# Kernel optimization log

Measured on AMD Instinct MI355X. Metric: run time of the kernel, lower is better.

## Reference

```python
import jax, jax.numpy as jnp
import numpy as np
from jax import lax

BN_EPS = 1e-5


def _conv(x, w):
    # stride-1, VALID conv; the torch 'locally connected' layer shares weights
    # across pixels, so it is exactly a standard conv2d.
    return lax.conv_general_dilated(
        x, w, window_strides=(1, 1), padding='VALID',
        dimension_numbers=('NCHW', 'OIHW', 'NCHW'))


def _batchnorm(x, gamma, beta):
    # training-mode BatchNorm2d: batch statistics over (N, H, W)
    mean = jnp.mean(x, axis=(0, 2, 3), keepdims=True)
    var = jnp.var(x, axis=(0, 2, 3), keepdims=True)
    xhat = (x - mean) * lax.rsqrt(var + BN_EPS)
    return xhat * gamma[None, :, None, None] + beta[None, :, None, None]


def setup_inputs() -> dict:
    key = jax.random.key(0)
    ks = jax.random.split(key, 6)
    B = 16384
    x = jax.random.normal(ks[0], (B, 256), dtype=jnp.float32)
    w1 = jax.random.normal(ks[1], (16, 1, 3, 3), dtype=jnp.float32)
    w2 = jax.random.normal(ks[2], (32, 16, 2, 2), dtype=jnp.float32)
    w3 = jax.random.normal(ks[3], (64, 32, 1, 1), dtype=jnp.float32)
    fan_in = 64 * 13 * 13
    bound = 1.0 / np.sqrt(fan_in)
    fc_w = jax.random.uniform(ks[4], (10, fan_in), minval=-bound, maxval=bound, dtype=jnp.float32)
    fc_b = jax.random.uniform(ks[5], (10,), minval=-bound, maxval=bound, dtype=jnp.float32)
    return {
        'x': x, 'w1': w1, 'w2': w2, 'w3': w3,
        'g1': jnp.ones((16,), jnp.float32), 'b1': jnp.zeros((16,), jnp.float32),
        'g2': jnp.ones((32,), jnp.float32), 'b2': jnp.zeros((32,), jnp.float32),
        'g3': jnp.ones((64,), jnp.float32), 'b3': jnp.zeros((64,), jnp.float32),
        'fc_w': fc_w, 'fc_b': fc_b,
    }


def reference(x, w1, w2, w3, g1, b1, g2, b2, g3, b3, fc_w, fc_b):
    h = x.reshape(-1, 1, 16, 16)                     # [B,1,16,16]
    h = jax.nn.relu(_batchnorm(_conv(h, w1), g1, b1))  # [B,16,14,14]
    h = jax.nn.relu(_batchnorm(_conv(h, w2), g2, b2))  # [B,32,13,13]
    h = jax.nn.relu(_batchnorm(_conv(h, w3), g3, b3))  # [B,64,13,13]
    h = h.reshape(h.shape[0], -1)                    # [B, 64*13*13]
    # dropout is identity in eval/deterministic mode
    return h @ fc_w.T + fc_b                         # [B,10]
```

## Files before the change

kernel.cpp:

```cpp
#include <hip/hip_runtime.h>


#define NPART 1024
#define P1_OFF 0
#define P2_OFF 32768
#define ST_OFF 229376
#define ST1 ST_OFF
#define ST2 (ST_OFF + 32)
#define ST3 (ST_OFF + 96)
#define C2R_OFF 230400
#define C2P_OFF 262144
#define A2G_BYTE 5242880ull
#define FCB_N (13 * 8192)
#define A1S 24
#define A1B 384
#define A3P 1048

typedef __attribute__((ext_vector_type(8))) short bf16x8;
typedef __attribute__((ext_vector_type(4))) float f32x4;

__device__ __forceinline__ unsigned int f2bf(float f) {
  unsigned int u = __float_as_uint(f);
  return (u + 0x7fffu + ((u >> 16) & 1u)) >> 16;
}
__device__ __forceinline__ unsigned int pkbf(float a, float b) {
  unsigned ua = __float_as_uint(a) + 0x8000u;
  unsigned ub = __float_as_uint(b) + 0x8000u;
  return __builtin_amdgcn_perm(ub, ua, 0x07060302u);
}
__device__ __forceinline__ short cvtbf(float a) {
  return (short)((__float_as_uint(a) + 0x8000u) >> 16);
}

__device__ __forceinline__ void conv1_mfma(
    const float* __restrict__ sxi,
    short* ph_buf,
    int r, int b, int q, bf16x8 b1f, float rs1, float rt1)
{
  bf16x8 af = {0, 0, 0, 0, 0, 0, 0, 0};
  unsigned* au = (unsigned*)&af;
  if (q == 0) {
    au[0] = pkbf(sxi[r * 16 + b],        sxi[r * 16 + b + 1]);
    au[1] = pkbf(sxi[r * 16 + b + 2],    sxi[(r + 1) * 16 + b]);
    au[2] = pkbf(sxi[(r + 1) * 16 + b + 1], sxi[(r + 1) * 16 + b + 2]);
    au[3] = pkbf(sxi[(r + 2) * 16 + b],  sxi[(r + 2) * 16 + b + 1]);
  } else if (q == 1) {
    au[0] = pkbf(sxi[(r + 2) * 16 + b + 2], 0.f);
  }
  f32x4 acc = {0.f, 0.f, 0.f, 0.f};
  acc = __builtin_amdgcn_mfma_f32_16x16x32_bf16(af, b1f, acc, 0, 0, 0);
  short* ph = ph_buf + (r & 1) * A1B;
#pragma unroll
  for (int rr = 0; rr < 4; ++rr) {
    float v = rs1 * acc[rr] + rt1;
    v = v > 0.f ? v : 0.f;
    ph[(4 * q + rr) * A1S + b] = cvtbf(v);
  }
}

__device__ __forceinline__ bf16x8 conv1_bfrag(const float* w1, int b, int q) {
  bf16x8 v;
#pragma unroll
  for (int j = 0; j < 8; ++j) {
    int tap = 8 * q + j;
    v[j] = (tap < 9) ? (short)f2bf(w1[b * 9 + tap]) : (short)0;
  }
  return v;
}

__global__ __launch_bounds__(256) void k1_xstats(
    const float* __restrict__ x, float* __restrict__ ws)
{
  __shared__ float sx[32 * 256];
  __shared__ float redl[4 * 56];
  const int tid = threadIdx.x, w = tid >> 6, lane = tid & 63;
  {
    const float4* xs = (const float4*)(x + (size_t)blockIdx.x * (32 * 256));
    float4* sd = (float4*)sx;
    for (int e = tid; e < 32 * 64; e += 256) sd[e] = xs[e];
  }
  __syncthreads();
  float S[9], C[45];
#pragma unroll
  for (int a = 0; a < 9; ++a) S[a] = 0.f;
#pragma unroll
  for (int a = 0; a < 45; ++a) C[a] = 0.f;
  for (int p = tid; p < 32 * 196; p += 256) {
    int img = p / 196, rem = p - img * 196;
    int i = rem / 14, j = rem - i * 14;
    const float* px = sx + img * 256 + i * 16 + j;
    float v[9];
    v[0] = px[0];  v[1] = px[1];  v[2] = px[2];
    v[3] = px[16]; v[4] = px[17]; v[5] = px[18];
    v[6] = px[32]; v[7] = px[33]; v[8] = px[34];
    int idx = 0;
#pragma unroll
    for (int a = 0; a < 9; ++a) {
      S[a] += v[a];
#pragma unroll
      for (int c = a; c < 9; ++c) { C[idx] += v[a] * v[c]; ++idx; }
    }
  }
#pragma unroll
  for (int a = 0; a < 9; ++a) {
    float v = S[a];
#pragma unroll
    for (int d = 1; d < 64; d <<= 1) v += __shfl_xor(v, d);
    if (lane == 0) redl[w * 56 + a] = v;
  }
#pragma unroll
  for (int a = 0; a < 45; ++a) {
    float v = C[a];
#pragma unroll
    for (int d = 1; d < 64; d <<= 1) v += __shfl_xor(v, d);
    if (lane == 0) redl[w * 56 + 9 + a] = v;
  }
  __syncthreads();
  if (tid < 54)
    ws[P1_OFF + blockIdx.x * 54 + tid] =
        redl[tid] + redl[56 + tid] + redl[112 + tid] + redl[168 + tid];
}

__global__ __launch_bounds__(256) void k_stats1(
    const float* __restrict__ w1, const float* __restrict__ gamma,
    const float* __restrict__ beta, float* __restrict__ ws)
{
  __shared__ float part[216];
  __shared__ float acc[54];
  const int tid = threadIdx.x;
  if (tid < 216) {
    int a = tid >> 2, seg = tid & 3;
    float s = 0.f;
    for (int i = seg * 128; i < seg * 128 + 128; ++i)
      s += ws[P1_OFF + i * 54 + a];
    part[tid] = s;
  }
  __syncthreads();
  if (tid < 54)
    acc[tid] = part[tid * 4] + part[tid * 4 + 1] +
               part[tid * 4 + 2] + part[tid * 4 + 3];
  __syncthreads();
  if (tid < 16) {
    float wr[9];
#pragma unroll
    for (int p = 0; p < 9; ++p) wr[p] = w1[tid * 9 + p];
    float msum = 0.f;
#pragma unroll
    for (int p = 0; p < 9; ++p) msum += wr[p] * acc[p];
    float e2 = 0.f;
    int idx = 9;
#pragma unroll
    for (int a = 0; a < 9; ++a)
#pragma unroll
      for (int c = a; c < 9; ++c) {
        float t = wr[a] * wr[c] * acc[idx];
        e2 += (c == a) ? t : 2.f * t;
        ++idx;
      }
    const float inv_n = 1.0f / (16384.0f * 196.0f);
    float mean = msum * inv_n;
    float var  = e2 * inv_n - mean * mean;
    float sv   = gamma[tid] * rsqrtf(var + 1e-5f);
    ws[ST1 + tid]      = sv;
    ws[ST1 + 16 + tid] = beta[tid] - mean * sv;
  }
}

__global__ __launch_bounds__(256) void k_stats2(
    const float* __restrict__ gamma, const float* __restrict__ beta,
    float* __restrict__ ws, int nch, int part_off, int st_off, float inv_n)
{
  const int c = blockIdx.x, tid = threadIdx.x;
  const int w = tid >> 6, lane = tid & 63;
  __shared__ float rs[4], rq[4];
  float s = 0.f, q = 0.f;
#pragma unroll 4
  for (int i = tid; i < NPART; i += 256) {
    s += ws[part_off + i * 2 * nch + c];
    q += ws[part_off + i * 2 * nch + nch + c];
  }
#pragma unroll
  for (int d = 1; d < 64; d <<= 1) {
    s += __shfl_xor(s, d);
    q += __shfl_xor(q, d);
  }
  if (lane == 0) { rs[w] = s; rq[w] = q; }
  __syncthreads();
  if (tid == 0) {
    float st = rs[0] + rs[1] + rs[2] + rs[3];
    float qt = rq[0] + rq[1] + rq[2] + rq[3];
    float mean = st * inv_n;
    float var  = qt * inv_n - mean * mean;
    float sv   = gamma[c] * rsqrtf(var + 1e-5f);
    ws[st_off + c]       = sv;
    ws[st_off + nch + c] = beta[c] - mean * sv;
  }
}

__global__ __launch_bounds__(256) void k3_conv2_stats(
    const float* __restrict__ x, const float* __restrict__ w1,
    const float* __restrict__ w2, float* __restrict__ ws)
{
  __shared__ float sx_s[16 * 256 + 16];
  __shared__ alignas(16) short a1h[4 * 2 * A1B];
  __shared__ float redf[256];
  const int tid = threadIdx.x, w = tid >> 6, lane = tid & 63;
  const int b = lane & 15, q = lane >> 4;
  {
    const float4* xs = (const float4*)(x + (size_t)blockIdx.x * (16 * 256));
    float4* sd = (float4*)sx_s;
    for (int e = tid; e < 16 * 64; e += 256) sd[e] = xs[e];
    if (tid < 16) sx_s[16 * 256 + tid] = 0.f;
  }
  bf16x8 b1f = conv1_bfrag(w1, b, q);
  const float rs1 = ws[ST1 + b], rt1 = ws[ST1 + 16 + b];
  bf16x8 b2h[4];
#pragma unroll
  for (int ks = 0; ks < 2; ++ks)
#pragma unroll
    for (int nt = 0; nt < 2; ++nt) {
      bf16x8 vh;
#pragma unroll
      for (int j = 0; j < 8; ++j) {
        int kk = 8 * (q & 1) + j, dj = q >> 1;
        vh[j] = (short)f2bf(w2[(nt * 16 + b) * 64 + kk * 4 + ks * 2 + dj]);
      }
      b2h[ks * 2 + nt] = vh;
    }
  float wm[4];
#pragma unroll
  for (int r = 0; r < 4; ++r) wm[r] = (4 * q + r) < 13 ? 1.f : 0.f;
  const int colAr = (b + (q >> 1) < 15) ? (b + (q >> 1)) : 15;
  const int offAl = colAr * A1S + 8 * (q & 1);
  __syncthreads();

  float s2[2] = {0.f, 0.f}, q2[2] = {0.f, 0.f};
  short* ph = a1h + w * (2 * A1B);
#pragma unroll 1
  for (int t = 0; t < 4; ++t) {
    const float* sxi = sx_s + (w * 4 + t) * 256;
    conv1_mfma(sxi, ph, 0, b, q, b1f, rs1, rt1);
    __builtin_amdgcn_wave_barrier();
#pragma unroll 1
    for (int i = 0; i < 13; ++i) {
      conv1_mfma(sxi, ph, i + 1, b, q, b1f, rs1, rt1);
      __builtin_amdgcn_wave_barrier();
      bf16x8 ah0 = *(const bf16x8*)(ph + (i & 1) * A1B + offAl);
      bf16x8 ah1 = *(const bf16x8*)(ph + ((i + 1) & 1) * A1B + offAl);
      f32x4 acc2[2] = {{0.f,0.f,0.f,0.f},{0.f,0.f,0.f,0.f}};
#pragma unroll
      for (int nt = 0; nt < 2; ++nt) {
        acc2[nt] = __builtin_amdgcn_mfma_f32_16x16x32_bf16(ah0, b2h[nt], acc2[nt], 0, 0, 0);
        acc2[nt] = __builtin_amdgcn_mfma_f32_16x16x32_bf16(ah1, b2h[2 + nt], acc2[nt], 0, 0, 0);
      }
#pragma unroll
      for (int nt = 0; nt < 2; ++nt)
#pragma unroll
        for (int r = 0; r < 4; ++r) {
          float ym = acc2[nt][r] * wm[r];
          s2[nt] += ym;
          q2[nt] = fmaf(ym, acc2[nt][r], q2[nt]);
        }
      __builtin_amdgcn_wave_barrier();
    }
  }
#pragma unroll
  for (int nt = 0; nt < 2; ++nt) {
    s2[nt] += __shfl_xor(s2[nt], 16); s2[nt] += __shfl_xor(s2[nt], 32);
    q2[nt] += __shfl_xor(q2[nt], 16); q2[nt] += __shfl_xor(q2[nt], 32);
  }
  if (lane < 16) {
    redf[w * 64 + b]      = s2[0];
    redf[w * 64 + 16 + b] = s2[1];
    redf[w * 64 + 32 + b] = q2[0];
    redf[w * 64 + 48 + b] = q2[1];
  }
  __syncthreads();
  if (tid < 64)
    ws[P2_OFF + blockIdx.x * 64 + tid] =
        redf[tid] + redf[64 + tid] + redf[128 + tid] + redf[192 + tid];
}

__global__ __launch_bounds__(256) void k5_a2(
    const float* __restrict__ x, const float* __restrict__ w1,
    const float* __restrict__ w2, float* __restrict__ ws,
    short* __restrict__ a2g, float* __restrict__ parts)
{
  __shared__ float sx_s[16 * 256 + 16];
  __shared__ alignas(16) short a1h[4 * 2 * A1B];
  __shared__ alignas(16) short a2w4[4 * 640];
  __shared__ alignas(16) short xt4[4 * 32 * 40];
  __shared__ float s2red[4 * 32];
  const int tid = threadIdx.x, w = tid >> 6, lane = tid & 63;
  const int b = lane & 15, q = lane >> 4;
  {
    const float4* xs = (const float4*)(x + (size_t)blockIdx.x * (16 * 256));
    float4* sd = (float4*)sx_s;
    for (int e = tid; e < 16 * 64; e += 256) sd[e] = xs[e];
    if (tid < 16) sx_s[16 * 256 + tid] = 0.f;
  }
  bf16x8 b1f = conv1_bfrag(w1, b, q);
  const float rs1 = ws[ST1 + b], rt1 = ws[ST1 + 16 + b];
  bf16x8 b2h[4];
#pragma unroll
  for (int ks = 0; ks < 2; ++ks)
#pragma unroll
    for (int nt = 0; nt < 2; ++nt) {
      bf16x8 vh;
#pragma unroll
      for (int j = 0; j < 8; ++j) {
        int kk = 8 * (q & 1) + j, dj = q >> 1;
        vh[j] = (short)f2bf(w2[(nt * 16 + b) * 64 + kk * 4 + ks * 2 + dj]);
      }
      b2h[ks * 2 + nt] = vh;
    }
  float rs2v[2], rt2v[2];
#pragma unroll
  for (int nt = 0; nt < 2; ++nt) {
    rs2v[nt] = ws[ST2 + nt * 16 + b];
    rt2v[nt] = ws[ST2 + 32 + nt * 16 + b];
  }
  float wm[4];
#pragma unroll
  for (int r = 0; r < 4; ++r) wm[r] = (4 * q + r) < 13 ? 1.f : 0.f;
  const int colAr = (b + (q >> 1) < 15) ? (b + (q >> 1)) : 15;
  const int offAl = colAr * A1S + 8 * (q & 1);
  short* a2w = a2w4 + w * 640;
  short* xt  = xt4 + w * 1280;
  __syncthreads();

  f32x4 accT0 = {0.f,0.f,0.f,0.f}, accT1 = {0.f,0.f,0.f,0.f},
        accT2 = {0.f,0.f,0.f,0.f};
  float s2a[2] = {0.f, 0.f};
  short* ph = a1h + w * (2 * A1B);
#pragma unroll 1
  for (int t = 0; t < 4; ++t) {
    const int img = blockIdx.x * 16 + w * 4 + t;
    const float* sxi = sx_s + (w * 4 + t) * 256;
    conv1_mfma(sxi, ph, 0, b, q, b1f, rs1, rt1);
    __builtin_amdgcn_wave_barrier();
#pragma unroll 1
    for (int i = 0; i < 13; ++i) {
      conv1_mfma(sxi, ph, i + 1, b, q, b1f, rs1, rt1);
      __builtin_amdgcn_wave_barrier();
      bf16x8 ah0 = *(const bf16x8*)(ph + (i & 1) * A1B + offAl);
      bf16x8 ah1 = *(const bf16x8*)(ph + ((i + 1) & 1) * A1B + offAl);
      f32x4 acc2[2] = {{0.f,0.f,0.f,0.f},{0.f,0.f,0.f,0.f}};
#pragma unroll
      for (int nt = 0; nt < 2; ++nt) {
        acc2[nt] = __builtin_amdgcn_mfma_f32_16x16x32_bf16(ah0, b2h[nt], acc2[nt], 0, 0, 0);
        acc2[nt] = __builtin_amdgcn_mfma_f32_16x16x32_bf16(ah1, b2h[2 + nt], acc2[nt], 0, 0, 0);
      }
#pragma unroll
      for (int nt = 0; nt < 2; ++nt) {
        float vm[4];
#pragma unroll
        for (int r = 0; r < 4; ++r) {
          float v = rs2v[nt] * acc2[nt][r] + rt2v[nt];
          v = v > 0.f ? v : 0.f;
          vm[r] = v * wm[r];
          a2w[(4 * q + r) * 40 + nt * 16 + b] = cvtbf(vm[r]);
        }
        uint2 pk2;
        pk2.x = pkbf(vm[0], vm[1]);
        pk2.y = pkbf(vm[2], vm[3]);
        *(uint2*)(xt + (nt * 16 + b) * 40 + (i & 1) * 16 + 4 * q) = pk2;
        s2a[nt] += (vm[0] + vm[1]) + (vm[2] + vm[3]);
      }
      __builtin_amdgcn_wave_barrier();
      {
        const unsigned* a2w32 = (const unsigned*)a2w;
        unsigned* a2g32 = (unsigned*)a2g;
        size_t dbase = (size_t)img * 2704 + (size_t)i * 208;
#pragma unroll
        for (int tt = 0; tt < 4; ++tt) {
          int f = tt * 64 + lane;
          if (f < 208) a2g32[dbase + f] = a2w32[(f >> 4) * 20 + (f & 15)];
        }
      }
      if (i & 1) {
        bf16x8 xf0 = *(const bf16x8*)(xt + b * 40 + 8 * q);
        bf16x8 xf1 = *(const bf16x8*)(xt + (16 + b) * 40 + 8 * q);
        accT0 = __builtin_amdgcn_mfma_f32_16x16x32_bf16(xf0, xf0, accT0, 0, 0, 0);
        accT1 = __builtin_amdgcn_mfma_f32_16x16x32_bf16(xf0, xf1, accT1, 0, 0, 0);
        accT2 = __builtin_amdgcn_mfma_f32_16x16x32_bf16(xf1, xf1, accT2, 0, 0, 0);
      }
      __builtin_amdgcn_wave_barrier();
    }
    {
      uint2 z; z.x = 0u; z.y = 0u;
      *(uint2*)(xt + b * 40 + 16 + 4 * q) = z;
      *(uint2*)(xt + (16 + b) * 40 + 16 + 4 * q) = z;
      __builtin_amdgcn_wave_barrier();
      bf16x8 xf0 = *(const bf16x8*)(xt + b * 40 + 8 * q);
      bf16x8 xf1 = *(const bf16x8*)(xt + (16 + b) * 40 + 8 * q);
      accT0 = __builtin_amdgcn_mfma_f32_16x16x32_bf16(xf0, xf0, accT0, 0, 0, 0);
      accT1 = __builtin_amdgcn_mfma_f32_16x16x32_bf16(xf0, xf1, accT1, 0, 0, 0);
      accT2 = __builtin_amdgcn_mfma_f32_16x16x32_bf16(xf1, xf1, accT2, 0, 0, 0);
      __builtin_amdgcn_wave_barrier();
    }
  }
#pragma unroll
  for (int nt = 0; nt < 2; ++nt) {
    s2a[nt] += __shfl_xor(s2a[nt], 16);
    s2a[nt] += __shfl_xor(s2a[nt], 32);
  }
  if (lane < 16) { s2red[w * 32 + b] = s2a[0]; s2red[w * 32 + 16 + b] = s2a[1]; }
  float* redc = sx_s;
#pragma unroll
  for (int rr = 0; rr < 4; ++rr) {
    int m = 4 * q + rr;
    redc[w * 1024 + 0   + m * 16 + b] = accT0[rr];
    redc[w * 1024 + 256 + m * 16 + b] = accT1[rr];
    redc[w * 1024 + 512 + m * 16 + b] = accT2[rr];
  }
  __syncthreads();
  for (int e = tid; e < 768; e += 256)
    parts[blockIdx.x * 800 + e] =
        redc[e] + redc[1024 + e] + redc[2048 + e] + redc[3072 + e];
  if (tid < 32)
    parts[blockIdx.x * 800 + 768 + tid] =
        s2red[tid] + s2red[32 + tid] + s2red[64 + tid] + s2red[96 + tid];
}

__global__ __launch_bounds__(256) void k_statsC(
    const float* __restrict__ parts, float* __restrict__ ws)
{
  const int e = blockIdx.x, tid = threadIdx.x;
  const int w = tid >> 6, lane = tid & 63;
  __shared__ float rs[4];
  float s = 0.f;
#pragma unroll 4
  for (int i = tid; i < 1024; i += 256) s += parts[i * 800 + e];
#pragma unroll
  for (int d = 1; d < 64; d <<= 1) s += __shfl_xor(s, d);
  if (lane == 0) rs[w] = s;
  __syncthreads();
  if (tid == 0) ws[C2R_OFF + e] = rs[0] + rs[1] + rs[2] + rs[3];
}

__global__ __launch_bounds__(64) void k_stats3n(
    const float* __restrict__ w3, const float* __restrict__ gamma,
    const float* __restrict__ beta, float* __restrict__ ws)
{
  const int c3 = threadIdx.x;
  if (c3 >= 64) return;
  const float* C2R = ws + C2R_OFF;
  float wr[32];
#pragma unroll
  for (int k = 0; k < 32; ++k) wr[k] = w3[c3 * 32 + k];
  const float inv_n = 1.0f / (16384.0f * 169.0f);
  float msum = 0.f;
#pragma unroll
  for (int k = 0; k < 32; ++k) msum += wr[k] * C2R[768 + k];
  float e2 = 0.f;
  for (int a = 0; a < 16; ++a)
#pragma unroll
    for (int bb = 0; bb < 16; ++bb) {
      e2 += wr[a] * wr[bb] * C2R[a * 16 + bb];
      e2 += wr[16 + a] * wr[16 + bb] * C2R[512 + a * 16 + bb];
      e2 += 2.f * wr[a] * wr[16 + bb] * C2R[256 + a * 16 + bb];
    }
  float mean = msum * inv_n;
  float var  = e2 * inv_n - mean * mean;
  float sv   = gamma[c3] * rsqrtf(var + 1e-5f);
  ws[ST3 + c3]      = sv;
  ws[ST3 + 64 + c3] = beta[c3] - mean * sv;
}

__global__ __launch_bounds__(256) void k0_fcB(
    const float* __restrict__ fcw, unsigned int* __restrict__ fcB)
{
  int F = blockIdx.x * 256 + threadIdx.x;
  if (F >= FCB_N) return;
  int u = F & 3, q = (F >> 2) & 3, jj = (F >> 4) & 15;
  int mm = (F >> 8) & 31, i = F >> 13;
  int k0 = mm * 32 + q * 8 + u * 2;
  unsigned lo = 0, hi = 0;
  if (jj < 10) {
    int c0 = k0 >> 4, j0 = k0 & 15;
    if (j0 < 13) lo = f2bf(fcw[jj * 10816 + c0 * 169 + i * 13 + j0]);
    int c1 = (k0 + 1) >> 4, j1 = (k0 + 1) & 15;
    if (j1 < 13) hi = f2bf(fcw[jj * 10816 + c1 * 169 + i * 13 + j1]);
  }
  fcB[F] = lo | (hi << 16);
}

__global__ __launch_bounds__(256) void k7_fc(
    const short* __restrict__ a2g, const float* __restrict__ w3,
    const float* __restrict__ fcb, const float* __restrict__ ws,
    float* __restrict__ out)
{
  __shared__ alignas(16) short a3buf[16 * A3P];
  const int tid = threadIdx.x, w = tid >> 6, lane = tid & 63;
  const int b = lane & 15, q = lane >> 4;
  bf16x8 b3h[4];
#pragma unroll
  for (int nt = 0; nt < 4; ++nt) {
    bf16x8 vh;
#pragma unroll
    for (int j = 0; j < 8; ++j)
      vh[j] = (short)f2bf(w3[(nt * 16 + b) * 32 + 8 * q + j]);
    b3h[nt] = vh;
  }
  float rs3v[4], rt3v[4], rs3z[4], rt3z[4];
#pragma unroll
  for (int nt = 0; nt < 4; ++nt) {
    rs3v[nt] = ws[ST3 + nt * 16 + b];
    rt3v[nt] = ws[ST3 + 64 + nt * 16 + b];
    rs3z[nt] = (q < 3) ? rs3v[nt] : 0.f;
    rt3z[nt] = (q < 3) ? rt3v[nt] : 0.f;
  }
  const bf16x8* fcB = (const bf16x8*)ws;
  f32x4 accF = {0.f, 0.f, 0.f, 0.f};
  const int pixc = (b < 12) ? b : 12;
  size_t ib[4];
#pragma unroll
  for (int t = 0; t < 4; ++t)
    ib[t] = (size_t)(blockIdx.x * 16 + w * 4 + t) * 5408;
  bf16x8 a2pre[4];
#pragma unroll
  for (int t = 0; t < 4; ++t)
    a2pre[t] = *(const bf16x8*)(a2g + ib[t] + pixc * 32 + 8 * q);

#pragma unroll 1
  for (int i = 0; i < 13; ++i) {
    bf16x8 a2cur[4];
#pragma unroll
    for (int t = 0; t < 4; ++t) a2cur[t] = a2pre[t];
    if (i < 12) {
#pragma unroll
      for (int t = 0; t < 4; ++t)
        a2pre[t] = *(const bf16x8*)(a2g + ib[t] +
                                    (size_t)((i + 1) * 13 + pixc) * 32 + 8 * q);
    }
#pragma unroll
    for (int t = 0; t < 4; ++t) {
      const int g = w * 4 + t;
#pragma unroll
      for (int nt = 0; nt < 4; ++nt) {
        f32x4 acc3 = {0.f, 0.f, 0.f, 0.f};
        acc3 = __builtin_amdgcn_mfma_f32_16x16x32_bf16(a2cur[t], b3h[nt], acc3, 0, 0, 0);
        float v0 = rs3v[nt] * acc3[0] + rt3v[nt];
        float v1 = rs3z[nt] * acc3[1] + rt3z[nt];
        float v2 = rs3z[nt] * acc3[2] + rt3z[nt];
        float v3 = rs3z[nt] * acc3[3] + rt3z[nt];
        v0 = v0 > 0.f ? v0 : 0.f;  v1 = v1 > 0.f ? v1 : 0.f;
        v2 = v2 > 0.f ? v2 : 0.f;  v3 = v3 > 0.f ? v3 : 0.f;
        uint2 pk2;
        pk2.x = pkbf(v0, v1);
        pk2.y = pkbf(v2, v3);
        *(uint2*)(a3buf + g * A3P + (nt * 16 + b) * 16 + 4 * q) = pk2;
      }
    }
    __syncthreads();
#pragma unroll
    for (int mm = 0; mm < 8; ++mm) {
      bf16x8 af = *(const bf16x8*)(a3buf + b * A3P + w * 256 + mm * 32 + 8 * q);
      bf16x8 bw = fcB[((i * 32 + w * 8 + mm) * 16 + b) * 4 + q];
      accF = __builtin_amdgcn_mfma_f32_16x16x32_bf16(af, bw, accF, 0, 0, 0);
    }
    __syncthreads();
  }

  float* redf7 = (float*)a3buf;
#pragma unroll
  for (int r = 0; r < 4; ++r)
    redf7[w * 256 + (4 * q + r) * 16 + b] = accF[r];
  __syncthreads();
  if (tid < 160) {
    int img = tid / 10, jj = tid - img * 10;
    float s = redf7[img * 16 + jj] + redf7[256 + img * 16 + jj] +
              redf7[512 + img * 16 + jj] + redf7[768 + img * 16 + jj];
    out[(blockIdx.x * 16 + img) * 10 + jj] = s + fcb[jj];
  }
}

extern "C" void kernel_launch(void* const* d_in, const int* in_sizes, int n_in,
                              void* d_out, int out_size, void* d_ws, size_t ws_size,
                              hipStream_t stream) {
  (void)in_sizes; (void)n_in; (void)out_size; (void)ws_size;
  const float* x   = (const float*)d_in[0];
  const float* w1  = (const float*)d_in[1];
  const float* w2  = (const float*)d_in[2];
  const float* w3  = (const float*)d_in[3];
  const float* g1  = (const float*)d_in[4];
  const float* b1  = (const float*)d_in[5];
  const float* g2  = (const float*)d_in[6];
  const float* b2  = (const float*)d_in[7];
  const float* g3  = (const float*)d_in[8];
  const float* b3  = (const float*)d_in[9];
  const float* fcw = (const float*)d_in[10];
  const float* fcb = (const float*)d_in[11];
  float* out = (float*)d_out;
  float* ws  = (float*)d_ws;
  short* a2g = (short*)((char*)d_ws + A2G_BYTE);
  float* parts = ws + C2P_OFF;

  k1_xstats<<<512, 256, 0, stream>>>(x, ws);
  k_stats1<<<1, 256, 0, stream>>>(w1, g1, b1, ws);
  k3_conv2_stats<<<1024, 256, 0, stream>>>(x, w1, w2, ws);
  k_stats2<<<32, 256, 0, stream>>>(g2, b2, ws, 32, P2_OFF, ST2,
                                   1.0f / (16384.0f * 169.0f));
  k5_a2<<<1024, 256, 0, stream>>>(x, w1, w2, ws, a2g, parts);
  k_statsC<<<800, 256, 0, stream>>>(parts, ws);
  k_stats3n<<<1, 64, 0, stream>>>(w3, g3, b3, ws);
  k0_fcB<<<FCB_N / 256, 256, 0, stream>>>(fcw, (unsigned int*)ws);
  k7_fc<<<1024, 256, 0, stream>>>(a2g, w3, fcb, ws, out);
}
```

Before: 296.5 us.

## Fold BN scale/shift into conv weights and MFMA accumulators; MFMA-based conv1 input Gram

Replaces the scalar per-thread 9x9 input covariance accumulation with an MFMA-based Gram (syrk) computation over patches plus a ones row, then reduces it with a new two-stage reduction. The BN scale is folded into the conv1/conv2/conv3 weights and the shift into the MFMA accumulator init, so the per-element FMA work after each MFMA is removed. Operand order for conv1/conv2 MFMAs is swapped so outputs are channel-major and can be stored packed, and conv2 activations are written to global directly instead of being staged through LDS. The trade-offs are bf16 rounding of the scaled weights, -1e30 sentinels used for masking, and an extra kernel launch.

New measurement: 278.9 us. -5.9%, faster.

```diff
diff --git a/kernel.cpp b/kernel.cpp
--- a/kernel.cpp
+++ b/kernel.cpp
@@ -2,13 +2,13 @@
 
 
 #define NPART 1024
-#define P1_OFF 0
 #define P2_OFF 32768
 #define ST_OFF 229376
 #define ST1 ST_OFF
 #define ST2 (ST_OFF + 32)
 #define ST3 (ST_OFF + 96)
 #define C2R_OFF 230400
+#define C1R_OFF 231424
 #define C2P_OFF 262144
 #define A2G_BYTE 5242880ull
 #define FCB_N (13 * 8192)
@@ -35,135 +35,137 @@
 __device__ __forceinline__ void conv1_mfma(
     const float* __restrict__ sxi,
     short* ph_buf,
-    int r, int b, int q, bf16x8 b1f, float rs1, float rt1)
-{
-  bf16x8 af = {0, 0, 0, 0, 0, 0, 0, 0};
-  unsigned* au = (unsigned*)&af;
+    int r, int b, int q, bf16x8 a1f, f32x4 c1i)
+{
+  bf16x8 bf = {0, 0, 0, 0, 0, 0, 0, 0};
+  unsigned* bu = (unsigned*)&bf;
   if (q == 0) {
-    au[0] = pkbf(sxi[r * 16 + b],        sxi[r * 16 + b + 1]);
-    au[1] = pkbf(sxi[r * 16 + b + 2],    sxi[(r + 1) * 16 + b]);
-    au[2] = pkbf(sxi[(r + 1) * 16 + b + 1], sxi[(r + 1) * 16 + b + 2]);
-    au[3] = pkbf(sxi[(r + 2) * 16 + b],  sxi[(r + 2) * 16 + b + 1]);
+    bu[0] = pkbf(sxi[r * 16 + b],           sxi[r * 16 + b + 1]);
+    bu[1] = pkbf(sxi[r * 16 + b + 2],       sxi[(r + 1) * 16 + b]);
+    bu[2] = pkbf(sxi[(r + 1) * 16 + b + 1], sxi[(r + 1) * 16 + b + 2]);
+    bu[3] = pkbf(sxi[(r + 2) * 16 + b],     sxi[(r + 2) * 16 + b + 1]);
   } else if (q == 1) {
-    au[0] = pkbf(sxi[(r + 2) * 16 + b + 2], 0.f);
-  }
-  f32x4 acc = {0.f, 0.f, 0.f, 0.f};
-  acc = __builtin_amdgcn_mfma_f32_16x16x32_bf16(af, b1f, acc, 0, 0, 0);
-  short* ph = ph_buf + (r & 1) * A1B;
-#pragma unroll
-  for (int rr = 0; rr < 4; ++rr) {
-    float v = rs1 * acc[rr] + rt1;
-    v = v > 0.f ? v : 0.f;
-    ph[(4 * q + rr) * A1S + b] = cvtbf(v);
-  }
-}
-
-__device__ __forceinline__ bf16x8 conv1_bfrag(const float* w1, int b, int q) {
+    bu[0] = pkbf(sxi[(r + 2) * 16 + b + 2], 0.f);
+  }
+  f32x4 acc = c1i;
+  acc = __builtin_amdgcn_mfma_f32_16x16x32_bf16(a1f, bf, acc, 0, 0, 0);
+  float v0 = acc[0] > 0.f ? acc[0] : 0.f;
+  float v1 = acc[1] > 0.f ? acc[1] : 0.f;
+  float v2 = acc[2] > 0.f ? acc[2] : 0.f;
+  float v3 = acc[3] > 0.f ? acc[3] : 0.f;
+  uint2 pk;
+  pk.x = pkbf(v0, v1);
+  pk.y = pkbf(v2, v3);
+  *(uint2*)(ph_buf + (r & 1) * A1B + b * A1S + 4 * q) = pk;
+}
+
+__device__ __forceinline__ bf16x8 conv1_afrag(const float* w1, float rs1b,
+                                              int b, int q) {
   bf16x8 v;
 #pragma unroll
   for (int j = 0; j < 8; ++j) {
     int tap = 8 * q + j;
-    v[j] = (tap < 9) ? (short)f2bf(w1[b * 9 + tap]) : (short)0;
+    v[j] = (tap < 9) ? (short)f2bf(w1[b * 9 + tap] * rs1b) : (short)0;
   }
   return v;
 }
 
-__global__ __launch_bounds__(256) void k1_xstats(
-    const float* __restrict__ x, float* __restrict__ ws)
-{
-  __shared__ float sx[32 * 256];
-  __shared__ float redl[4 * 56];
+__global__ __launch_bounds__(256) void k1_xsyrk(
+    const float* __restrict__ x, float* __restrict__ parts)
+{
+  __shared__ float sx[16 * 256];
   const int tid = threadIdx.x, w = tid >> 6, lane = tid & 63;
+  const int b = lane & 15, q = lane >> 4;
   {
-    const float4* xs = (const float4*)(x + (size_t)blockIdx.x * (32 * 256));
+    const float4* xs = (const float4*)(x + (size_t)blockIdx.x * (16 * 256));
     float4* sd = (float4*)sx;
-    for (int e = tid; e < 32 * 64; e += 256) sd[e] = xs[e];
-  }
-  __syncthreads();
-  float S[9], C[45];
-#pragma unroll
-  for (int a = 0; a < 9; ++a) S[a] = 0.f;
-#pragma unroll
-  for (int a = 0; a < 45; ++a) C[a] = 0.f;
-  for (int p = tid; p < 32 * 196; p += 256) {
-    int img = p / 196, rem = p - img * 196;
-    int i = rem / 14, j = rem - i * 14;
-    const float* px = sx + img * 256 + i * 16 + j;
-    float v[9];
-    v[0] = px[0];  v[1] = px[1];  v[2] = px[2];
-    v[3] = px[16]; v[4] = px[17]; v[5] = px[18];
-    v[6] = px[32]; v[7] = px[33]; v[8] = px[34];
-    int idx = 0;
-#pragma unroll
-    for (int a = 0; a < 9; ++a) {
-      S[a] += v[a];
-#pragma unroll
-      for (int c = a; c < 9; ++c) { C[idx] += v[a] * v[c]; ++idx; }
-    }
-  }
-#pragma unroll
-  for (int a = 0; a < 9; ++a) {
-    float v = S[a];
-#pragma unroll
-    for (int d = 1; d < 64; d <<= 1) v += __shfl_xor(v, d);
-    if (lane == 0) redl[w * 56 + a] = v;
-  }
-#pragma unroll
-  for (int a = 0; a < 45; ++a) {
-    float v = C[a];
-#pragma unroll
-    for (int d = 1; d < 64; d <<= 1) v += __shfl_xor(v, d);
-    if (lane == 0) redl[w * 56 + 9 + a] = v;
-  }
-  __syncthreads();
-  if (tid < 54)
-    ws[P1_OFF + blockIdx.x * 54 + tid] =
-        redl[tid] + redl[56 + tid] + redl[112 + tid] + redl[168 + tid];
-}
-
-__global__ __launch_bounds__(256) void k_stats1(
+    for (int e = tid; e < 16 * 64; e += 256) sd[e] = xs[e];
+  }
+  __syncthreads();
+  const int di = (b < 9) ? (b / 3) : 0;
+  const int dj = (b < 9) ? (b - di * 3) : 0;
+  const int h = q >> 1, jb = (q & 1) * 8;
+  f32x4 acc = {0.f, 0.f, 0.f, 0.f};
+#pragma unroll 1
+  for (int t = 0; t < 4; ++t) {
+    const float* sxi = sx + (w * 4 + t) * 256;
+#pragma unroll 1
+    for (int s = 0; s < 7; ++s) {
+      bf16x8 af;
+      unsigned* au = (unsigned*)&af;
+      if (b < 9) {
+        const float* srow = sxi + (2 * s + h + di) * 16 + dj;
+#pragma unroll
+        for (int cc = 0; cc < 4; ++cc) {
+          float v0 = (jb + 2 * cc     < 14) ? srow[jb + 2 * cc]     : 0.f;
+          float v1 = (jb + 2 * cc + 1 < 14) ? srow[jb + 2 * cc + 1] : 0.f;
+          au[cc] = pkbf(v0, v1);
+        }
+      } else if (b == 9) {
+#pragma unroll
+        for (int cc = 0; cc < 4; ++cc) {
+          unsigned lo = (jb + 2 * cc     < 14) ? 0x3F80u : 0u;
+          unsigned hi = (jb + 2 * cc + 1 < 14) ? 0x3F800000u : 0u;
+          au[cc] = lo | hi;
+        }
+      } else {
+#pragma unroll
+        for (int cc = 0; cc < 4; ++cc) au[cc] = 0u;
+      }
+      acc = __builtin_amdgcn_mfma_f32_16x16x32_bf16(af, af, acc, 0, 0, 0);
+    }
+  }
+  __syncthreads();
+  float* redc = sx;
+#pragma unroll
+  for (int rr = 0; rr < 4; ++rr)
+    redc[w * 256 + (4 * q + rr) * 16 + b] = acc[rr];
+  __syncthreads();
+  parts[blockIdx.x * 256 + tid] =
+      redc[tid] + redc[256 + tid] + redc[512 + tid] + redc[768 + tid];
+}
+
+__global__ __launch_bounds__(256) void k_stats1a(
+    const float* __restrict__ parts, float* __restrict__ ws)
+{
+  const int e = blockIdx.x, tid = threadIdx.x;
+  const int w = tid >> 6, lane = tid & 63;
+  __shared__ float rs[4];
+  float s = 0.f;
+#pragma unroll 4
+  for (int i = tid; i < 1024; i += 256) s += parts[i * 256 + e];
+#pragma unroll
+  for (int d = 1; d < 64; d <<= 1) s += __shfl_xor(s, d);
+  if (lane == 0) rs[w] = s;
+  __syncthreads();
+  if (tid == 0) ws[C1R_OFF + e] = rs[0] + rs[1] + rs[2] + rs[3];
+}
+
+__global__ __launch_bounds__(64) void k_stats1b(
     const float* __restrict__ w1, const float* __restrict__ gamma,
     const float* __restrict__ beta, float* __restrict__ ws)
 {
-  __shared__ float part[216];
-  __shared__ float acc[54];
-  const int tid = threadIdx.x;
-  if (tid < 216) {
-    int a = tid >> 2, seg = tid & 3;
-    float s = 0.f;
-    for (int i = seg * 128; i < seg * 128 + 128; ++i)
-      s += ws[P1_OFF + i * 54 + a];
-    part[tid] = s;
-  }
-  __syncthreads();
-  if (tid < 54)
-    acc[tid] = part[tid * 4] + part[tid * 4 + 1] +
-               part[tid * 4 + 2] + part[tid * 4 + 3];
-  __syncthreads();
-  if (tid < 16) {
-    float wr[9];
-#pragma unroll
-    for (int p = 0; p < 9; ++p) wr[p] = w1[tid * 9 + p];
-    float msum = 0.f;
-#pragma unroll
-    for (int p = 0; p < 9; ++p) msum += wr[p] * acc[p];
-    float e2 = 0.f;
-    int idx = 9;
-#pragma unroll
-    for (int a = 0; a < 9; ++a)
-#pragma unroll
-      for (int c = a; c < 9; ++c) {
-        float t = wr[a] * wr[c] * acc[idx];
-        e2 += (c == a) ? t : 2.f * t;
-        ++idx;
-      }
-    const float inv_n = 1.0f / (16384.0f * 196.0f);
-    float mean = msum * inv_n;
-    float var  = e2 * inv_n - mean * mean;
-    float sv   = gamma[tid] * rsqrtf(var + 1e-5f);
-    ws[ST1 + tid]      = sv;
-    ws[ST1 + 16 + tid] = beta[tid] - mean * sv;
-  }
+  const int c = threadIdx.x;
+  if (c >= 16) return;
+  const float* C = ws + C1R_OFF;
+  float wr[9];
+#pragma unroll
+  for (int p = 0; p < 9; ++p) wr[p] = w1[c * 9 + p];
+  float msum = 0.f;
+#pragma unroll
+  for (int p = 0; p < 9; ++p) msum += wr[p] * C[9 * 16 + p];
+  float e2 = 0.f;
+#pragma unroll
+  for (int a = 0; a < 9; ++a)
+#pragma unroll
+    for (int bb = 0; bb < 9; ++bb)
+      e2 += wr[a] * wr[bb] * C[a * 16 + bb];
+  const float inv_n = 1.0f / (16384.0f * 196.0f);
+  float mean = msum * inv_n;
+  float var  = e2 * inv_n - mean * mean;
+  float sv   = gamma[c] * rsqrtf(var + 1e-5f);
+  ws[ST1 + c]      = sv;
+  ws[ST1 + 16 + c] = beta[c] - mean * sv;
 }
 
 __global__ __launch_bounds__(256) void k_stats2(
@@ -212,8 +214,10 @@
     for (int e = tid; e < 16 * 64; e += 256) sd[e] = xs[e];
     if (tid < 16) sx_s[16 * 256 + tid] = 0.f;
   }
-  bf16x8 b1f = conv1_bfrag(w1, b, q);
-  const float rs1 = ws[ST1 + b], rt1 = ws[ST1 + 16 + b];
+  bf16x8 a1f = conv1_afrag(w1, ws[ST1 + b], b, q);
+  f32x4 c1i;
+#pragma unroll
+  for (int r = 0; r < 4; ++r) c1i[r] = ws[ST1 + 16 + 4 * q + r];
   bf16x8 b2h[4];
 #pragma unroll
   for (int ks = 0; ks < 2; ++ks)
@@ -227,54 +231,56 @@
       }
       b2h[ks * 2 + nt] = vh;
     }
-  float wm[4];
-#pragma unroll
-  for (int r = 0; r < 4; ++r) wm[r] = (4 * q + r) < 13 ? 1.f : 0.f;
+  const float vb = (b < 13) ? 1.f : 0.f;
   const int colAr = (b + (q >> 1) < 15) ? (b + (q >> 1)) : 15;
   const int offAl = colAr * A1S + 8 * (q & 1);
   __syncthreads();
 
-  float s2[2] = {0.f, 0.f}, q2[2] = {0.f, 0.f};
+  float s2r[2][4] = {{0.f,0.f,0.f,0.f},{0.f,0.f,0.f,0.f}};
+  float q2r[2][4] = {{0.f,0.f,0.f,0.f},{0.f,0.f,0.f,0.f}};
   short* ph = a1h + w * (2 * A1B);
 #pragma unroll 1
   for (int t = 0; t < 4; ++t) {
     const float* sxi = sx_s + (w * 4 + t) * 256;
-    conv1_mfma(sxi, ph, 0, b, q, b1f, rs1, rt1);
+    conv1_mfma(sxi, ph, 0, b, q, a1f, c1i);
     __builtin_amdgcn_wave_barrier();
 #pragma unroll 1
     for (int i = 0; i < 13; ++i) {
-      conv1_mfma(sxi, ph, i + 1, b, q, b1f, rs1, rt1);
+      conv1_mfma(sxi, ph, i + 1, b, q, a1f, c1i);
       __builtin_amdgcn_wave_barrier();
       bf16x8 ah0 = *(const bf16x8*)(ph + (i & 1) * A1B + offAl);
       bf16x8 ah1 = *(const bf16x8*)(ph + ((i + 1) & 1) * A1B + offAl);
       f32x4 acc2[2] = {{0.f,0.f,0.f,0.f},{0.f,0.f,0.f,0.f}};
 #pragma unroll
       for (int nt = 0; nt < 2; ++nt) {
-        acc2[nt] = __builtin_amdgcn_mfma_f32_16x16x32_bf16(ah0, b2h[nt], acc2[nt], 0, 0, 0);
-        acc2[nt] = __builtin_amdgcn_mfma_f32_16x16x32_bf16(ah1, b2h[2 + nt], acc2[nt], 0, 0, 0);
+        acc2[nt] = __builtin_amdgcn_mfma_f32_16x16x32_bf16(b2h[nt], ah0, acc2[nt], 0, 0, 0);
+        acc2[nt] = __builtin_amdgcn_mfma_f32_16x16x32_bf16(b2h[2 + nt], ah1, acc2[nt], 0, 0, 0);
       }
 #pragma unroll
       for (int nt = 0; nt < 2; ++nt)
 #pragma unroll
         for (int r = 0; r < 4; ++r) {
-          float ym = acc2[nt][r] * wm[r];
-          s2[nt] += ym;
-          q2[nt] = fmaf(ym, acc2[nt][r], q2[nt]);
+          float ym = acc2[nt][r] * vb;
+          s2r[nt][r] += ym;
+          q2r[nt][r] = fmaf(ym, acc2[nt][r], q2r[nt][r]);
         }
       __builtin_amdgcn_wave_barrier();
     }
   }
 #pragma unroll
-  for (int nt = 0; nt < 2; ++nt) {
-    s2[nt] += __shfl_xor(s2[nt], 16); s2[nt] += __shfl_xor(s2[nt], 32);
-    q2[nt] += __shfl_xor(q2[nt], 16); q2[nt] += __shfl_xor(q2[nt], 32);
-  }
-  if (lane < 16) {
-    redf[w * 64 + b]      = s2[0];
-    redf[w * 64 + 16 + b] = s2[1];
-    redf[w * 64 + 32 + b] = q2[0];
-    redf[w * 64 + 48 + b] = q2[1];
-  }
+  for (int nt = 0; nt < 2; ++nt)
+#pragma unroll
+    for (int r = 0; r < 4; ++r) {
+      float sv = s2r[nt][r], qv = q2r[nt][r];
+      sv += __shfl_xor(sv, 1); sv += __shfl_xor(sv, 2);
+      sv += __shfl_xor(sv, 4); sv += __shfl_xor(sv, 8);
+      qv += __shfl_xor(qv, 1); qv += __shfl_xor(qv, 2);
+      qv += __shfl_xor(qv, 4); qv += __shfl_xor(qv, 8);
+      if (b == 0) {
+        redf[w * 64 + nt * 16 + 4 * q + r]      = sv;
+        redf[w * 64 + 32 + nt * 16 + 4 * q + r] = qv;
+      }
+    }
   __syncthreads();
   if (tid < 64)
     ws[P2_OFF + blockIdx.x * 64 + tid] =
@@ -288,7 +294,6 @@
 {
   __shared__ float sx_s[16 * 256 + 16];
   __shared__ alignas(16) short a1h[4 * 2 * A1B];
-  __shared__ alignas(16) short a2w4[4 * 640];
   __shared__ alignas(16) short xt4[4 * 32 * 40];
   __shared__ float s2red[4 * 32];
   const int tid = threadIdx.x, w = tid >> 6, lane = tid & 63;
@@ -299,85 +304,72 @@
     for (int e = tid; e < 16 * 64; e += 256) sd[e] = xs[e];
     if (tid < 16) sx_s[16 * 256 + tid] = 0.f;
   }
-  bf16x8 b1f = conv1_bfrag(w1, b, q);
-  const float rs1 = ws[ST1 + b], rt1 = ws[ST1 + 16 + b];
+  bf16x8 a1f = conv1_afrag(w1, ws[ST1 + b], b, q);
+  f32x4 c1i;
+#pragma unroll
+  for (int r = 0; r < 4; ++r) c1i[r] = ws[ST1 + 16 + 4 * q + r];
   bf16x8 b2h[4];
 #pragma unroll
   for (int ks = 0; ks < 2; ++ks)
 #pragma unroll
     for (int nt = 0; nt < 2; ++nt) {
+      float rs2b = ws[ST2 + nt * 16 + b];
       bf16x8 vh;
 #pragma unroll
       for (int j = 0; j < 8; ++j) {
         int kk = 8 * (q & 1) + j, dj = q >> 1;
-        vh[j] = (short)f2bf(w2[(nt * 16 + b) * 64 + kk * 4 + ks * 2 + dj]);
+        vh[j] = (short)f2bf(w2[(nt * 16 + b) * 64 + kk * 4 + ks * 2 + dj] * rs2b);
       }
       b2h[ks * 2 + nt] = vh;
     }
-  float rs2v[2], rt2v[2];
-#pragma unroll
-  for (int nt = 0; nt < 2; ++nt) {
-    rs2v[nt] = ws[ST2 + nt * 16 + b];
-    rt2v[nt] = ws[ST2 + 32 + nt * 16 + b];
-  }
-  float wm[4];
-#pragma unroll
-  for (int r = 0; r < 4; ++r) wm[r] = (4 * q + r) < 13 ? 1.f : 0.f;
+  f32x4 c2i[2];
+#pragma unroll
+  for (int nt = 0; nt < 2; ++nt)
+#pragma unroll
+    for (int r = 0; r < 4; ++r)
+      c2i[nt][r] = (b < 13) ? ws[ST2 + 32 + nt * 16 + 4 * q + r] : -1e30f;
   const int colAr = (b + (q >> 1) < 15) ? (b + (q >> 1)) : 15;
   const int offAl = colAr * A1S + 8 * (q & 1);
-  short* a2w = a2w4 + w * 640;
-  short* xt  = xt4 + w * 1280;
+  short* xt = xt4 + w * 1280;
   __syncthreads();
 
   f32x4 accT0 = {0.f,0.f,0.f,0.f}, accT1 = {0.f,0.f,0.f,0.f},
         accT2 = {0.f,0.f,0.f,0.f};
-  float s2a[2] = {0.f, 0.f};
+  float s2aR[2][4] = {{0.f,0.f,0.f,0.f},{0.f,0.f,0.f,0.f}};
   short* ph = a1h + w * (2 * A1B);
 #pragma unroll 1
   for (int t = 0; t < 4; ++t) {
     const int img = blockIdx.x * 16 + w * 4 + t;
     const float* sxi = sx_s + (w * 4 + t) * 256;
-    conv1_mfma(sxi, ph, 0, b, q, b1f, rs1, rt1);
+    conv1_mfma(sxi, ph, 0, b, q, a1f, c1i);
     __builtin_amdgcn_wave_barrier();
 #pragma unroll 1
     for (int i = 0; i < 13; ++i) {
-      conv1_mfma(sxi, ph, i + 1, b, q, b1f, rs1, rt1);
+      conv1_mfma(sxi, ph, i + 1, b, q, a1f, c1i);
       __builtin_amdgcn_wave_barrier();
       bf16x8 ah0 = *(const bf16x8*)(ph + (i & 1) * A1B + offAl);
       bf16x8 ah1 = *(const bf16x8*)(ph + ((i + 1) & 1) * A1B + offAl);
-      f32x4 acc2[2] = {{0.f,0.f,0.f,0.f},{0.f,0.f,0.f,0.f}};
 #pragma unroll
       for (int nt = 0; nt < 2; ++nt) {
-        acc2[nt] = __builtin_amdgcn_mfma_f32_16x16x32_bf16(ah0, b2h[nt], acc2[nt], 0, 0, 0);
-        acc2[nt] = __builtin_amdgcn_mfma_f32_16x16x32_bf16(ah1, b2h[2 + nt], acc2[nt], 0, 0, 0);
-      }
-#pragma unroll
-      for (int nt = 0; nt < 2; ++nt) {
+        f32x4 acc2 = c2i[nt];
+        acc2 = __builtin_amdgcn_mfma_f32_16x16x32_bf16(b2h[nt], ah0, acc2, 0, 0, 0);
+        acc2 = __builtin_amdgcn_mfma_f32_16x16x32_bf16(b2h[2 + nt], ah1, acc2, 0, 0, 0);
         float vm[4];
 #pragma unroll
         for (int r = 0; r < 4; ++r) {
-          float v = rs2v[nt] * acc2[nt][r] + rt2v[nt];
-          v = v > 0.f ? v : 0.f;
-          vm[r] = v * wm[r];
-          a2w[(4 * q + r) * 40 + nt * 16 + b] = cvtbf(vm[r]);
+          vm[r] = acc2[r] > 0.f ? acc2[r] : 0.f;
+          s2aR[nt][r] += vm[r];
+          xt[(nt * 16 + 4 * q + r) * 40 + (i & 1) * 16 + b] = cvtbf(vm[r]);
         }
-        uint2 pk2;
-        pk2.x = pkbf(vm[0], vm[1]);
-        pk2.y = pkbf(vm[2], vm[3]);
-        *(uint2*)(xt + (nt * 16 + b) * 40 + (i & 1) * 16 + 4 * q) = pk2;
-        s2a[nt] += (vm[0] + vm[1]) + (vm[2] + vm[3]);
+        if (b < 13) {
+          uint2 pk;
+          pk.x = pkbf(vm[0], vm[1]);
+          pk.y = pkbf(vm[2], vm[3]);
+          *(uint2*)(a2g + (size_t)img * 5408 + (size_t)(i * 13 + b) * 32 +
+                    nt * 16 + 4 * q) = pk;
+        }
       }
       __builtin_amdgcn_wave_barrier();
-      {
-        const unsigned* a2w32 = (const unsigned*)a2w;
-        unsigned* a2g32 = (unsigned*)a2g;
-        size_t dbase = (size_t)img * 2704 + (size_t)i * 208;
-#pragma unroll
-        for (int tt = 0; tt < 4; ++tt) {
-          int f = tt * 64 + lane;
-          if (f < 208) a2g32[dbase + f] = a2w32[(f >> 4) * 20 + (f & 15)];
-        }
-      }
       if (i & 1) {
         bf16x8 xf0 = *(const bf16x8*)(xt + b * 40 + 8 * q);
         bf16x8 xf1 = *(const bf16x8*)(xt + (16 + b) * 40 + 8 * q);
@@ -401,11 +393,14 @@
     }
   }
 #pragma unroll
-  for (int nt = 0; nt < 2; ++nt) {
-    s2a[nt] += __shfl_xor(s2a[nt], 16);
-    s2a[nt] += __shfl_xor(s2a[nt], 32);
-  }
-  if (lane < 16) { s2red[w * 32 + b] = s2a[0]; s2red[w * 32 + 16 + b] = s2a[1]; }
+  for (int nt = 0; nt < 2; ++nt)
+#pragma unroll
+    for (int r = 0; r < 4; ++r) {
+      float sv = s2aR[nt][r];
+      sv += __shfl_xor(sv, 1); sv += __shfl_xor(sv, 2);
+      sv += __shfl_xor(sv, 4); sv += __shfl_xor(sv, 8);
+      if (b == 0) s2red[w * 32 + nt * 16 + 4 * q + r] = sv;
+    }
   float* redc = sx_s;
 #pragma unroll
   for (int rr = 0; rr < 4; ++rr) {
@@ -495,21 +490,20 @@
   const int tid = threadIdx.x, w = tid >> 6, lane = tid & 63;
   const int b = lane & 15, q = lane >> 4;
   bf16x8 b3h[4];
+  f32x4 c3i[4];
 #pragma unroll
   for (int nt = 0; nt < 4; ++nt) {
+    float s3 = ws[ST3 + nt * 16 + b];
+    float t3 = ws[ST3 + 64 + nt * 16 + b];
     bf16x8 vh;
 #pragma unroll
     for (int j = 0; j < 8; ++j)
-      vh[j] = (short)f2bf(w3[(nt * 16 + b) * 32 + 8 * q + j]);
+      vh[j] = (short)f2bf(w3[(nt * 16 + b) * 32 + 8 * q + j] * s3);
     b3h[nt] = vh;
-  }
-  float rs3v[4], rt3v[4], rs3z[4], rt3z[4];
-#pragma unroll
-  for (int nt = 0; nt < 4; ++nt) {
-    rs3v[nt] = ws[ST3 + nt * 16 + b];
-    rt3v[nt] = ws[ST3 + 64 + nt * 16 + b];
-    rs3z[nt] = (q < 3) ? rs3v[nt] : 0.f;
-    rt3z[nt] = (q < 3) ? rt3v[nt] : 0.f;
+    c3i[nt][0] = t3;
+#pragma unroll
+    for (int r = 1; r < 4; ++r)
+      c3i[nt][r] = (q < 3) ? t3 : -1e30f;
   }
   const bf16x8* fcB = (const bf16x8*)ws;
   f32x4 accF = {0.f, 0.f, 0.f, 0.f};
@@ -539,14 +533,12 @@
       const int g = w * 4 + t;
 #pragma unroll
       for (int nt = 0; nt < 4; ++nt) {
-        f32x4 acc3 = {0.f, 0.f, 0.f, 0.f};
+        f32x4 acc3 = c3i[nt];
         acc3 = __builtin_amdgcn_mfma_f32_16x16x32_bf16(a2cur[t], b3h[nt], acc3, 0, 0, 0);
-        float v0 = rs3v[nt] * acc3[0] + rt3v[nt];
-        float v1 = rs3z[nt] * acc3[1] + rt3z[nt];
-        float v2 = rs3z[nt] * acc3[2] + rt3z[nt];
-        float v3 = rs3z[nt] * acc3[3] + rt3z[nt];
-        v0 = v0 > 0.f ? v0 : 0.f;  v1 = v1 > 0.f ? v1 : 0.f;
-        v2 = v2 > 0.f ? v2 : 0.f;  v3 = v3 > 0.f ? v3 : 0.f;
+        float v0 = acc3[0] > 0.f ? acc3[0] : 0.f;
+        float v1 = acc3[1] > 0.f ? acc3[1] : 0.f;
+        float v2 = acc3[2] > 0.f ? acc3[2] : 0.f;
+        float v3 = acc3[3] > 0.f ? acc3[3] : 0.f;
         uint2 pk2;
         pk2.x = pkbf(v0, v1);
         pk2.y = pkbf(v2, v3);
@@ -597,8 +589,9 @@
   short* a2g = (short*)((char*)d_ws + A2G_BYTE);
   float* parts = ws + C2P_OFF;
 
-  k1_xstats<<<512, 256, 0, stream>>>(x, ws);
-  k_stats1<<<1, 256, 0, stream>>>(w1, g1, b1, ws);
+  k1_xsyrk<<<1024, 256, 0, stream>>>(x, parts);
+  k_stats1a<<<256, 256, 0, stream>>>(parts, ws);
+  k_stats1b<<<1, 64, 0, stream>>>(w1, g1, b1, ws);
   k3_conv2_stats<<<1024, 256, 0, stream>>>(x, w1, w2, ws);
   k_stats2<<<32, 256, 0, stream>>>(g2, b2, ws, 32, P2_OFF, ST2,
                                    1.0f / (16384.0f * 169.0f));
```
